# Kernel optimization log

Hardware: AMD Instinct MI355X
Metric: run time of the kernel (lower is better)

Reference implementation:

```python
import jax, jax.numpy as jnp
import numpy as np

B, A, C, M = 8, 120000, 9, 64
ALPHA, GAMMA = 0.25, 2.0


def setup_inputs() -> dict:
    key = jax.random.key(0)
    k1, k2, k3, k4, k5, k6, k7 = jax.random.split(key, 7)
    # anchors: plausible rotated boxes [x1,y1,x2,y2,angle]
    cx = jax.random.uniform(k1, (A,), minval=0.0, maxval=1024.0)
    cy = jax.random.uniform(k2, (A,), minval=0.0, maxval=1024.0)
    w = jax.random.uniform(k3, (A,), minval=16.0, maxval=128.0)
    h = jax.random.uniform(k4, (A,), minval=16.0, maxval=128.0)
    ang = jax.random.uniform(k5, (A,), minval=0.0, maxval=np.pi)
    anchor = jnp.stack([cx - 0.5 * w, cy - 0.5 * h, cx + 0.5 * w, cy + 0.5 * h, ang], axis=1)
    anchors = anchor[None]  # [1, A, 5]
    # annotations: copies of distinct anchor boxes -> guaranteed IoU=1 matches
    idx = jnp.arange(B * M).reshape(B, M)  # disjoint anchor indices per image
    boxes = anchor[idx]  # [B, M, 5]
    cls_col = jax.random.randint(k6, (B, M), 1, 4).astype(jnp.float32)  # class in {1,2,3} < C
    flag = jnp.zeros((B, M, 1), jnp.float32)  # valid (!= -1)
    annotations = jnp.concatenate([boxes[..., :4], cls_col[..., None], flag], axis=-1)  # [B, M, 6]
    classifications = jax.random.uniform(k7, (B, A, C), minval=0.0, maxval=1.0)
    regressions = jax.random.normal(jax.random.fold_in(key, 9), (B, A, 5)) * 0.1
    return {
        "classifications": classifications,
        "regressions": regressions,
        "anchors": anchors,
        "annotations": annotations,
    }


def _per_image(cls_p, reg, ann, anchor):
    # cls_p: [A,C], reg: [A,5], ann: [M,6], anchor: [A,5]
    valid = ann[:, 5] != -1.0
    has_ann = jnp.any(valid)
    p = jnp.clip(cls_p, 1e-4, 1.0 - 1e-4)
    a, b = anchor, ann[:, :5]
    # pairwise rotated IoU (arIoU)  [A, M]
    iw = jnp.clip(jnp.minimum(a[:, 2, None], b[None, :, 2]) - jnp.maximum(a[:, 0, None], b[None, :, 0]), 0.0)
    ih = jnp.clip(jnp.minimum(a[:, 3, None], b[None, :, 3]) - jnp.maximum(a[:, 1, None], b[None, :, 1]), 0.0)
    area_a = (a[:, 2] - a[:, 0]) * (a[:, 3] - a[:, 1])
    area_b = (b[:, 2] - b[:, 0]) * (b[:, 3] - b[:, 1])
    inter = iw * ih
    ua = jnp.clip(area_a[:, None] + area_b[None, :] - inter, 1e-8)
    iou = inter / ua
    ariou = iou * jnp.cos(jnp.abs(a[:, 4, None] - b[None, :, 4]) - np.pi / 2)
    ariou = jnp.where(valid[None, :], ariou, -1e9)  # mask invalid annotations
    iou_max = ariou.max(axis=1)
    iou_arg = ariou.argmax(axis=1)
    assigned = ann[iou_arg]  # [A, 6]
    pos = iou_max >= 0.5
    neg = iou_max < 0.4
    num_pos = pos.sum().astype(p.dtype)
    # targets: -1 = ignore, one-hot for positives, 0 for negatives
    cls_idx = assigned[:, 4].astype(jnp.int32)
    onehot = jax.nn.one_hot(cls_idx, p.shape[1], dtype=p.dtype)
    targets = jnp.where(pos[:, None], onehot, jnp.where(neg[:, None], 0.0, -1.0))
    # focal BCE
    alpha_factor = jnp.where(targets == 1.0, ALPHA, 1.0 - ALPHA)
    focal_weight = alpha_factor * jnp.where(targets == 1.0, 1.0 - p, p) ** GAMMA
    ce = -(targets * jnp.log(p) + (1.0 - targets) * jnp.log(1.0 - p))
    cls_loss = jnp.where(targets != -1.0, focal_weight * ce, 0.0).sum() / jnp.maximum(num_pos, 1.0)
    aw = a[:, 2] - a[:, 0]
    ah = a[:, 3] - a[:, 1]
    acx = a[:, 0] + 0.5 * aw
    acy = a[:, 1] + 0.5 * ah
    gw_raw = assigned[:, 2] - assigned[:, 0]
    gh_raw = assigned[:, 3] - assigned[:, 1]
    gcx = assigned[:, 0] + 0.5 * gw_raw
    gcy = assigned[:, 1] + 0.5 * gh_raw
    gw = jnp.clip(gw_raw, 1.0)
    gh = jnp.clip(gh_raw, 1.0)
    t = jnp.stack(
        [(gcx - acx) / aw, (gcy - acy) / ah, jnp.log(gw / aw), jnp.log(gh / ah), jnp.tan(assigned[:, 4] - a[:, 4])],
        axis=1,
    ) / jnp.array([[0.1, 0.1, 0.2, 0.2, 1.0]], dtype=p.dtype)
    diff = jnp.abs(t - reg)
    sl1 = jnp.where(diff <= 1.0 / 9.0, 0.5 * 9.0 * diff * diff, diff - 0.5 / 9.0)
    reg_loss = jnp.where(num_pos > 0.0, (sl1 * pos[:, None]).sum() / jnp.maximum(num_pos * 5.0, 1.0), 0.0)
    cls_loss = jnp.where(has_ann, cls_loss, 0.0)
    reg_loss = jnp.where(has_ann, reg_loss, 0.0)
    return cls_loss, reg_loss


def reference(classifications, regressions, anchors, annotations):
    anchor = anchors[0]
    cls_l, reg_l = jax.vmap(_per_image, in_axes=(0, 0, 0, None))(classifications, regressions, annotations, anchor)
    return cls_l.mean(keepdims=True), reg_l.mean(keepdims=True)
```

## Files before the change

kernel.cpp:

```cpp
#include <hip/hip_runtime.h>
#include <math.h>


constexpr int Bn = 8, An = 120000, Cn = 9, Mn = 64;
constexpr int R = 2;
constexpr int TPB = 256;
constexpr int APB = TPB * R;
constexpr int GX = (An + APB - 1) / APB;

typedef float f4 __attribute__((ext_vector_type(4), aligned(4)));
typedef float f2 __attribute__((ext_vector_type(2), aligned(4)));

__global__ __launch_bounds__(TPB) void focal_main(
    const float* __restrict__ cls,
    const float* __restrict__ reg,
    const float* __restrict__ anchors,
    const float* __restrict__ ann,
    float* __restrict__ ws)
{
    __shared__ float4 sT[Mn][2];
    __shared__ float sred[4][3];

    const int tid = threadIdx.x;
    const int b = blockIdx.y;
    const int base = blockIdx.x * APB + tid;

    if (tid < Mn) {
        const float* a6 = ann + ((size_t)b * Mn + tid) * 6;
        f4 v0 = *(const f4*)a6;
        f2 v1 = *(const f2*)(a6 + 4);
        float x1 = v0.x, y1 = v0.y, x2 = v0.z, y2 = v0.w, cv = v1.x;
        float sb, cb;
        sincosf(cv, &sb, &cb);
        if (v1.y == -1.0f) { x1 = y1 = x2 = y2 = 0.f; sb = cb = 0.f; cv = 0.f; }
        sT[tid][0] = make_float4(x1, y1, x2, y2);
        sT[tid][1] = make_float4(sb, cb, (x2 - x1) * (y2 - y1), cv);
    }
    __syncthreads();

    float ax1[R], ay1[R], ax2[R], ay2[R], areaA[R], sa[R], ca[R], aangv[R];
    float bestA[R], bestB[R];
    int bestK[R];
    bool act[R];
    f4 c0[R], c1[R];
    float c8[R];

    #pragma unroll
    for (int r = 0; r < R; ++r) {
        const int i = base + r * TPB;
        act[r] = (i < An);
        const int ii = act[r] ? i : (An - 1);
        bestA[r] = 0.f; bestB[r] = 1.f; bestK[r] = 0;
        const float* a5 = anchors + (size_t)ii * 5;
        f4 av5 = *(const f4*)a5;
        ax1[r] = av5.x; ay1[r] = av5.y; ax2[r] = av5.z; ay2[r] = av5.w;
        aangv[r] = a5[4];
        areaA[r] = (ax2[r] - ax1[r]) * (ay2[r] - ay1[r]);
        sincosf(aangv[r], &sa[r], &ca[r]);
        const float* pc = cls + ((size_t)b * An + ii) * (size_t)Cn;
        c0[r] = *(const f4*)pc;
        c1[r] = *(const f4*)(pc + 4);
        c8[r] = pc[8];
    }

    #pragma unroll 4
    for (int k = 0; k < Mn; ++k) {
        const float4 bx = sT[k][0];
        const float4 au = sT[k][1];
        #pragma unroll
        for (int r = 0; r < R; ++r) {
            float iw = fminf(ax2[r], bx.z) - fmaxf(ax1[r], bx.x);
            float ih = fminf(ay2[r], bx.w) - fmaxf(ay1[r], bx.y);
            iw = fmaxf(iw, 0.f); ih = fmaxf(ih, 0.f);
            float inter = iw * ih;
            float ua = fmaxf(areaA[r] + au.z - inter, 1e-8f);
            float s = fabsf(sa[r] * au.y - ca[r] * au.x);
            float av = inter * s;
            bool upd = (av * bestB[r] > bestA[r] * ua);
            bestA[r] = upd ? av : bestA[r];
            bestB[r] = upd ? ua : bestB[r];
            bestK[r] = upd ? k : bestK[r];
        }
    }

    float csum = 0.f, rsum = 0.f, pcnt = 0.f;

    #pragma unroll
    for (int r = 0; r < R; ++r) {
        if (!act[r]) continue;
        const int i = base + r * TPB;
        const bool pos = bestA[r] >= 0.5f * bestB[r];
        const bool neg = bestA[r] <  0.4f * bestB[r];

        if (pos || neg) {
            const float4 au = sT[bestK[r]][1];
            const int ci = (int)au.w;
            float pv[9] = { c0[r].x, c0[r].y, c0[r].z, c0[r].w,
                            c1[r].x, c1[r].y, c1[r].z, c1[r].w, c8[r] };
            #pragma unroll
            for (int c = 0; c < Cn; ++c) {
                float p = fminf(fmaxf(pv[c], 1e-4f), 0.9999f);
                bool hit = pos && (c == ci);
                float t = hit ? (1.f - p) : p;
                float m = hit ? p : (1.f - p);
                float w = hit ? 0.25f : 0.75f;
                csum += w * t * t * (-__logf(m));
            }
        }

        if (pos) {
            pcnt += 1.f;
            const float4 gb = sT[bestK[r]][0];
            const float4 au = sT[bestK[r]][1];
            float aw = ax2[r] - ax1[r], ah = ay2[r] - ay1[r];
            float acx = ax1[r] + 0.5f * aw, acy = ay1[r] + 0.5f * ah;
            float gwr = gb.z - gb.x, ghr = gb.w - gb.y;
            float gcx = gb.x + 0.5f * gwr, gcy = gb.y + 0.5f * ghr;
            float gw = fmaxf(gwr, 1.f), gh = fmaxf(ghr, 1.f);
            float tt[5];
            tt[0] = ((gcx - acx) / aw) * 10.f;
            tt[1] = ((gcy - acy) / ah) * 10.f;
            tt[2] = logf(gw / aw) * 5.f;
            tt[3] = logf(gh / ah) * 5.f;
            tt[4] = tanf(au.w - aangv[r]);
            const float* rg = reg + ((size_t)b * An + i) * 5;
            #pragma unroll
            for (int j = 0; j < 5; ++j) {
                float d = fabsf(tt[j] - rg[j]);
                rsum += (d <= (1.f / 9.f)) ? (4.5f * d * d) : (d - (0.5f / 9.f));
            }
        }
    }

    #pragma unroll
    for (int off = 32; off > 0; off >>= 1) {
        csum += __shfl_down(csum, off, 64);
        rsum += __shfl_down(rsum, off, 64);
        pcnt += __shfl_down(pcnt, off, 64);
    }
    const int wave = tid >> 6;
    if ((tid & 63) == 0) {
        sred[wave][0] = csum; sred[wave][1] = rsum; sred[wave][2] = pcnt;
    }
    __syncthreads();
    if (tid == 0) {
        float c = sred[0][0] + sred[1][0] + sred[2][0] + sred[3][0];
        float r = sred[0][1] + sred[1][1] + sred[2][1] + sred[3][1];
        float p = sred[0][2] + sred[1][2] + sred[2][2] + sred[3][2];
        const int j = b * GX + blockIdx.x;
        ws[j * 4 + 0] = c;
        ws[j * 4 + 1] = r;
        ws[j * 4 + 2] = p;
    }
}

__global__ __launch_bounds__(512) void focal_final(
    const float* __restrict__ ann,
    const float* __restrict__ ws,
    float* __restrict__ out)
{
    __shared__ float simg[Bn][2];
    const int tid = threadIdx.x;
    const int w = tid >> 6;
    const int lane = tid & 63;

    float c = 0.f, r = 0.f, p = 0.f;
    for (int j = lane; j < GX; j += 64) {
        const int idx = (w * GX + j) * 4;
        c += ws[idx + 0]; r += ws[idx + 1]; p += ws[idx + 2];
    }
    float fl = ann[((size_t)w * Mn + lane) * 6 + 5];
    bool has = __any(fl != -1.0f);

    #pragma unroll
    for (int off = 32; off > 0; off >>= 1) {
        c += __shfl_down(c, off, 64);
        r += __shfl_down(r, off, 64);
        p += __shfl_down(p, off, 64);
    }
    if (lane == 0) {
        float cl = 0.f, rl = 0.f;
        if (has) {
            cl = c / fmaxf(p, 1.f);
            rl = (p > 0.f) ? r / fmaxf(p * 5.f, 1.f) : 0.f;
        }
        simg[w][0] = cl; simg[w][1] = rl;
    }
    __syncthreads();
    if (tid == 0) {
        float cl = 0.f, rl = 0.f;
        #pragma unroll
        for (int b = 0; b < Bn; ++b) { cl += simg[b][0]; rl += simg[b][1]; }
        out[0] = cl / (float)Bn;
        out[1] = rl / (float)Bn;
    }
}

extern "C" void kernel_launch(void* const* d_in, const int* in_sizes, int n_in,
                              void* d_out, int out_size, void* d_ws, size_t ws_size,
                              hipStream_t stream) {
    const float* cls     = (const float*)d_in[0];
    const float* reg     = (const float*)d_in[1];
    const float* anchors = (const float*)d_in[2];
    const float* ann     = (const float*)d_in[3];
    float* out = (float*)d_out;
    float* ws  = (float*)d_ws;

    dim3 grid(GX, Bn);
    focal_main<<<grid, TPB, 0, stream>>>(cls, reg, anchors, ann, ws);
    focal_final<<<1, 512, 0, stream>>>(ann, ws, out);
}
```

Baseline: 127.5 us.

## Precompute annotation tile in prep kernel and defer classification loads

Moves the per-block annotation preprocessing (sincos, masking, area) into a separate single-block prep kernel that writes a global tile. The main kernel then reads that tile with uniform vector loads instead of building shared memory and synchronising. Classification loads move from before the IoU loop to after it, which lowers register pressure but puts those loads back on the critical path. The focal loss is also split into specialised positive and negative branches. The cost is an extra kernel launch, and the uniform loads rely on the scalar or L1 cache.

```diff
diff --git a/kernel.cpp b/kernel.cpp
--- a/kernel.cpp
+++ b/kernel.cpp
@@ -7,43 +7,48 @@
 constexpr int TPB = 256;
 constexpr int APB = TPB * R;
 constexpr int GX = (An + APB - 1) / APB;
+constexpr int TILE_F = Bn * Mn * 8;
 
 typedef float f4 __attribute__((ext_vector_type(4), aligned(4)));
 typedef float f2 __attribute__((ext_vector_type(2), aligned(4)));
+typedef float f8v __attribute__((ext_vector_type(8), aligned(32)));
+
+__global__ __launch_bounds__(Bn * Mn) void focal_prep(
+    const float* __restrict__ ann, float* __restrict__ tile)
+{
+    const int t = threadIdx.x;
+    const int b = t >> 6, m = t & 63;
+    const float* a6 = ann + ((size_t)b * Mn + m) * 6;
+    f4 v0 = *(const f4*)a6;
+    f2 v1 = *(const f2*)(a6 + 4);
+    float x1 = v0.x, y1 = v0.y, x2 = v0.z, y2 = v0.w, cv = v1.x;
+    float sb, cb;
+    sincosf(cv, &sb, &cb);
+    if (v1.y == -1.0f) { x1 = y1 = x2 = y2 = 0.f; sb = cb = 0.f; cv = 0.f; }
+    f8v o;
+    o[0] = x1; o[1] = y1; o[2] = x2; o[3] = y2;
+    o[4] = sb; o[5] = cb; o[6] = (x2 - x1) * (y2 - y1); o[7] = cv;
+    *(f8v*)(tile + (size_t)t * 8) = o;
+}
 
 __global__ __launch_bounds__(TPB) void focal_main(
     const float* __restrict__ cls,
     const float* __restrict__ reg,
     const float* __restrict__ anchors,
-    const float* __restrict__ ann,
-    float* __restrict__ ws)
+    const float* __restrict__ tile,
+    float* __restrict__ part)
 {
-    __shared__ float4 sT[Mn][2];
     __shared__ float sred[4][3];
 
     const int tid = threadIdx.x;
     const int b = blockIdx.y;
     const int base = blockIdx.x * APB + tid;
-
-    if (tid < Mn) {
-        const float* a6 = ann + ((size_t)b * Mn + tid) * 6;
-        f4 v0 = *(const f4*)a6;
-        f2 v1 = *(const f2*)(a6 + 4);
-        float x1 = v0.x, y1 = v0.y, x2 = v0.z, y2 = v0.w, cv = v1.x;
-        float sb, cb;
-        sincosf(cv, &sb, &cb);
-        if (v1.y == -1.0f) { x1 = y1 = x2 = y2 = 0.f; sb = cb = 0.f; cv = 0.f; }
-        sT[tid][0] = make_float4(x1, y1, x2, y2);
-        sT[tid][1] = make_float4(sb, cb, (x2 - x1) * (y2 - y1), cv);
-    }
-    __syncthreads();
+    const float* Tb = tile + (size_t)b * Mn * 8;
 
     float ax1[R], ay1[R], ax2[R], ay2[R], areaA[R], sa[R], ca[R], aangv[R];
     float bestA[R], bestB[R];
     int bestK[R];
     bool act[R];
-    f4 c0[R], c1[R];
-    float c8[R];
 
     #pragma unroll
     for (int r = 0; r < R; ++r) {
@@ -57,24 +62,19 @@
         aangv[r] = a5[4];
         areaA[r] = (ax2[r] - ax1[r]) * (ay2[r] - ay1[r]);
         sincosf(aangv[r], &sa[r], &ca[r]);
-        const float* pc = cls + ((size_t)b * An + ii) * (size_t)Cn;
-        c0[r] = *(const f4*)pc;
-        c1[r] = *(const f4*)(pc + 4);
-        c8[r] = pc[8];
     }
 
     #pragma unroll 4
     for (int k = 0; k < Mn; ++k) {
-        const float4 bx = sT[k][0];
-        const float4 au = sT[k][1];
+        const f8v t = *(const f8v*)(Tb + k * 8);
         #pragma unroll
         for (int r = 0; r < R; ++r) {
-            float iw = fminf(ax2[r], bx.z) - fmaxf(ax1[r], bx.x);
-            float ih = fminf(ay2[r], bx.w) - fmaxf(ay1[r], bx.y);
+            float iw = fminf(ax2[r], t[2]) - fmaxf(ax1[r], t[0]);
+            float ih = fminf(ay2[r], t[3]) - fmaxf(ay1[r], t[1]);
             iw = fmaxf(iw, 0.f); ih = fmaxf(ih, 0.f);
             float inter = iw * ih;
-            float ua = fmaxf(areaA[r] + au.z - inter, 1e-8f);
-            float s = fabsf(sa[r] * au.y - ca[r] * au.x);
+            float ua = fmaxf(areaA[r] + t[6] - inter, 1e-8f);
+            float s = fabsf(sa[r] * t[5] - ca[r] * t[4]);
             float av = inter * s;
             bool upd = (av * bestB[r] > bestA[r] * ua);
             bestA[r] = upd ? av : bestA[r];
@@ -91,27 +91,23 @@
         const int i = base + r * TPB;
         const bool pos = bestA[r] >= 0.5f * bestB[r];
         const bool neg = bestA[r] <  0.4f * bestB[r];
-
-        if (pos || neg) {
-            const float4 au = sT[bestK[r]][1];
-            const int ci = (int)au.w;
-            float pv[9] = { c0[r].x, c0[r].y, c0[r].z, c0[r].w,
-                            c1[r].x, c1[r].y, c1[r].z, c1[r].w, c8[r] };
+        const float* pc = cls + ((size_t)b * An + i) * (size_t)Cn;
+
+        if (pos) {
+            pcnt += 1.f;
+            const float* g = Tb + (size_t)bestK[r] * 8;
+            f4 gb = *(const f4*)g;
+            f4 g2 = *(const f4*)(g + 4);
+            const int ci = (int)g2.w;
             #pragma unroll
             for (int c = 0; c < Cn; ++c) {
-                float p = fminf(fmaxf(pv[c], 1e-4f), 0.9999f);
-                bool hit = pos && (c == ci);
+                float p = fminf(fmaxf(pc[c], 1e-4f), 0.9999f);
+                bool hit = (c == ci);
                 float t = hit ? (1.f - p) : p;
                 float m = hit ? p : (1.f - p);
                 float w = hit ? 0.25f : 0.75f;
                 csum += w * t * t * (-__logf(m));
             }
-        }
-
-        if (pos) {
-            pcnt += 1.f;
-            const float4 gb = sT[bestK[r]][0];
-            const float4 au = sT[bestK[r]][1];
             float aw = ax2[r] - ax1[r], ah = ay2[r] - ay1[r];
             float acx = ax1[r] + 0.5f * aw, acy = ay1[r] + 0.5f * ah;
             float gwr = gb.z - gb.x, ghr = gb.w - gb.y;
@@ -122,13 +118,19 @@
             tt[1] = ((gcy - acy) / ah) * 10.f;
             tt[2] = logf(gw / aw) * 5.f;
             tt[3] = logf(gh / ah) * 5.f;
-            tt[4] = tanf(au.w - aangv[r]);
+            tt[4] = tanf(g2.w - aangv[r]);
             const float* rg = reg + ((size_t)b * An + i) * 5;
             #pragma unroll
             for (int j = 0; j < 5; ++j) {
                 float d = fabsf(tt[j] - rg[j]);
                 rsum += (d <= (1.f / 9.f)) ? (4.5f * d * d) : (d - (0.5f / 9.f));
             }
+        } else if (neg) {
+            #pragma unroll
+            for (int c = 0; c < Cn; ++c) {
+                float p = fminf(fmaxf(pc[c], 1e-4f), 0.9999f);
+                csum += 0.75f * p * p * (-__logf(1.f - p));
+            }
         }
     }
 
@@ -148,15 +150,15 @@
         float r = sred[0][1] + sred[1][1] + sred[2][1] + sred[3][1];
         float p = sred[0][2] + sred[1][2] + sred[2][2] + sred[3][2];
         const int j = b * GX + blockIdx.x;
-        ws[j * 4 + 0] = c;
-        ws[j * 4 + 1] = r;
-        ws[j * 4 + 2] = p;
+        part[j * 4 + 0] = c;
+        part[j * 4 + 1] = r;
+        part[j * 4 + 2] = p;
     }
 }
 
 __global__ __launch_bounds__(512) void focal_final(
     const float* __restrict__ ann,
-    const float* __restrict__ ws,
+    const float* __restrict__ part,
     float* __restrict__ out)
 {
     __shared__ float simg[Bn][2];
@@ -167,7 +169,7 @@
     float c = 0.f, r = 0.f, p = 0.f;
     for (int j = lane; j < GX; j += 64) {
         const int idx = (w * GX + j) * 4;
-        c += ws[idx + 0]; r += ws[idx + 1]; p += ws[idx + 2];
+        c += part[idx + 0]; r += part[idx + 1]; p += part[idx + 2];
     }
     float fl = ann[((size_t)w * Mn + lane) * 6 + 5];
     bool has = __any(fl != -1.0f);
@@ -204,9 +206,12 @@
     const float* anchors = (const float*)d_in[2];
     const float* ann     = (const float*)d_in[3];
     float* out = (float*)d_out;
-    float* ws  = (float*)d_ws;
-
+    float* wsf = (float*)d_ws;
+    float* tile = wsf;
+    float* part = wsf + TILE_F;
+
+    focal_prep<<<1, Bn * Mn, 0, stream>>>(ann, tile);
     dim3 grid(GX, Bn);
-    focal_main<<<grid, TPB, 0, stream>>>(cls, reg, anchors, ann, ws);
-    focal_final<<<1, 512, 0, stream>>>(ann, ws, out);
-}
+    focal_main<<<grid, TPB, 0, stream>>>(cls, reg, anchors, tile, part);
+    focal_final<<<1, 512, 0, stream>>>(ann, part, out);
+}
```

New measurement: 130.7 us. 2.5% more time.
